# Performance work log

Hardware: AMD Instinct MI355X
Metric: run time of the kernel (lower is better)

Reference implementation:

```python
import jax, jax.numpy as jnp
import numpy as np


def _gcn_conv(x, src, dst, W, b, n_nodes):
    """PyG GCNConv: out = D^-1/2 (A+I) D^-1/2 (x @ W) + b, sym norm with self-loops."""
    loop = jnp.arange(n_nodes, dtype=src.dtype)
    s = jnp.concatenate([src, loop])  # sources incl self-loops
    d = jnp.concatenate([dst, loop])  # destinations incl self-loops
    ones = jnp.ones(d.shape[0], dtype=x.dtype)
    deg = jax.ops.segment_sum(ones, d, num_segments=n_nodes)
    dinv = jnp.where(deg > 0, jax.lax.rsqrt(deg), 0.0)
    norm = dinv[s] * dinv[d]  # [E+N]
    h = x @ W  # dense transform first (in>=out channels), [N, H]
    msg = h[s] * norm[:, None]  # gather + scale, [E+N, H]
    out = jax.ops.segment_sum(msg, d, num_segments=n_nodes)  # scatter-add
    return out + b


def setup_inputs() -> dict:
    N, E, C_IN, C_H = 50000, 640000, 128, 128
    key = jax.random.key(0)
    k_x, k_e, k_w1, k_w2 = jax.random.split(key, 4)
    x = jax.random.normal(k_x, (N, C_IN), dtype=jnp.float32)
    edge_index = jax.random.randint(k_e, (2, E), 0, N, dtype=jnp.int64)
    # Glorot-style init for GCN weights, zero bias (PyG defaults)
    W1 = jax.random.normal(k_w1, (C_IN, C_H), dtype=jnp.float32) * (1.0 / np.sqrt(C_IN))
    b1 = jnp.zeros((C_H,), dtype=jnp.float32)
    W2 = jax.random.normal(k_w2, (C_H, C_H), dtype=jnp.float32) * (1.0 / np.sqrt(C_H))
    b2 = jnp.zeros((C_H,), dtype=jnp.float32)
    return {"x": x, "edge_index": edge_index, "W1": W1, "b1": b1, "W2": W2, "b2": b2}


def reference(x, edge_index, W1, b1, W2, b2):
    n_nodes = x.shape[0]
    src, dst = edge_index[0], edge_index[1]
    h = jax.nn.relu(_gcn_conv(x, src, dst, W1, b1, n_nodes))
    # dropout p=0.5 is identity in eval mode (training=False)
    h = jax.nn.relu(_gcn_conv(h, src, dst, W2, b2, n_nodes))
    return h
```

## Files before the change

### kernel.cpp

```cpp
#include <hip/hip_runtime.h>
#include <hip/hip_bf16.h>
#include <cstdint>

#define CH 128
#define NB 512
#define SCHUNK 4096

typedef __attribute__((ext_vector_type(8))) short short8;
typedef __attribute__((ext_vector_type(4))) float f32x4;

union FragU {
  uint4 u;
  short8 s;
  ushort h[8];
};

__device__ __forceinline__ float bf_lo(uint32_t u) { return __uint_as_float(u << 16); }
__device__ __forceinline__ float bf_hi(uint32_t u) { return __uint_as_float(u & 0xffff0000u); }
__device__ __forceinline__ uint32_t f2bf(float f) {
  uint32_t u = __float_as_uint(f);
  u += 0x7fff + ((u >> 16) & 1);
  return u >> 16;
}

__global__ __launch_bounds__(256) void k_histw(const int* __restrict__ dst, int* __restrict__ counts,
                                               int E, int nblk,
                                               const float* __restrict__ W1, const float* __restrict__ W2,
                                               ushort* __restrict__ wbuf) {
  int blk = blockIdx.x;
  if (blk >= nblk) {
    int bb = blk - nblk;
    int which = bb >> 6;
    int idx = (bb & 63) * 256 + threadIdx.x;
    const float* W = which ? W2 : W1;
    ushort* hi = wbuf + which * 32768;
    ushort* lo = hi + 16384;
    int k = idx >> 7, n = idx & 127;
    float w = W[idx];
    uint32_t hb = f2bf(w);
    uint32_t lb = f2bf(w - bf_lo(hb));
    int j = n >> 4, t = k >> 5, ln = (n & 15) | (((k >> 3) & 3) << 4), i = k & 7;
    int p = (j * 4 + t) * 512 + ln * 8 + i;
    hi[p] = (ushort)hb;
    lo[p] = (ushort)lb;
    return;
  }
  __shared__ int sh[NB];
  int t = threadIdx.x;
  for (int i = t; i < NB; i += 256) sh[i] = 0;
  __syncthreads();
  int base = blk * SCHUNK, lim = min(base + SCHUNK, E);
  for (int i = base + t; i < lim; i += 256) atomicAdd(&sh[dst[i] >> 7], 1);
  __syncthreads();
  for (int i = t; i < NB; i += 256) counts[i * nblk + blk] = sh[i];
}

__global__ __launch_bounds__(1024) void k_scan1(const int* __restrict__ in, int* __restrict__ excl,
                                                int* __restrict__ blocksum, int n) {
  __shared__ int sd[1024];
  int tid = threadIdx.x;
  int i = blockIdx.x * 1024 + tid;
  int v = (i < n) ? in[i] : 0;
  int x = v;
  sd[tid] = x;
  __syncthreads();
  for (int off = 1; off < 1024; off <<= 1) {
    int t = (tid >= off) ? sd[tid - off] : 0;
    __syncthreads();
    x += t;
    sd[tid] = x;
    __syncthreads();
  }
  if (i < n) excl[i] = x - v;
  if (tid == 1023) blocksum[blockIdx.x] = x;
}

__global__ void k_scan2b(int* __restrict__ bs, int nb) {
  __shared__ int sh[128];
  int t = threadIdx.x;
  int v = (t < nb) ? bs[t] : 0;
  sh[t] = v;
  __syncthreads();
  for (int off = 1; off < 128; off <<= 1) {
    int add = (t >= off) ? sh[t - off] : 0;
    __syncthreads();
    sh[t] += add;
    __syncthreads();
  }
  if (t < nb) bs[t] = sh[t] - v;
}

__global__ __launch_bounds__(256) void k_scan3b(int* __restrict__ excl, const int* __restrict__ boff,
                                                int* __restrict__ bbase, int total, int nblk, int E) {
  int i = blockIdx.x * 256 + threadIdx.x;
  if (i < total) {
    int val = excl[i] + boff[i >> 10];
    excl[i] = val;
    if (i % nblk == 0) bbase[i / nblk] = val;
  }
  if (i == 0) bbase[NB] = E;
}

__global__ __launch_bounds__(256) void k_scatter3(const int* __restrict__ src, const int* __restrict__ dst,
                                                  const int* __restrict__ excl, uint32_t* __restrict__ packed,
                                                  int E, int nblk) {
  __shared__ int lcur[NB];
  int t = threadIdx.x, blk = blockIdx.x;
  for (int i = t; i < NB; i += 256) lcur[i] = excl[i * nblk + blk];
  __syncthreads();
  int base = blk * SCHUNK, lim = min(base + SCHUNK, E);
  for (int i = base + t; i < lim; i += 256) {
    int d = dst[i], s = src[i];
    int slot = atomicAdd(&lcur[d >> 7], 1);
    packed[slot] = (uint32_t)s | ((uint32_t)(d & 127) << 16);
  }
}

__global__ __launch_bounds__(256) void k_bucket(const uint32_t* __restrict__ packed, const int* __restrict__ bbase,
                                                int* __restrict__ csr_src, int* __restrict__ row_ptr,
                                                float* __restrict__ dinv, int N, int E, int nb) {
  __shared__ int hist[128];
  __shared__ int scan[128];
  __shared__ int cur[128];
  int b = blockIdx.x;
  int t = threadIdx.x;
  int base = bbase[b], end = bbase[b + 1];
  if (t < 128) hist[t] = 0;
  __syncthreads();
  for (int i = base + t; i < end; i += 256)
    atomicAdd(&hist[packed[i] >> 16], 1);
  __syncthreads();
  int v = (t < 128) ? hist[t] : 0;
  if (t < 128) scan[t] = v;
  __syncthreads();
  for (int off = 1; off < 128; off <<= 1) {
    int add = (t < 128 && t >= off) ? scan[t - off] : 0;
    __syncthreads();
    if (t < 128) scan[t] += add;
    __syncthreads();
  }
  if (t < 128) {
    int excl = scan[t] - v;
    cur[t] = excl;
    int node = b * 128 + t;
    if (node < N) {
      row_ptr[node] = base + excl;
      dinv[node] = rsqrtf((float)(v + 1));
    }
    if (b == nb - 1 && t == 0) row_ptr[N] = E;
  }
  __syncthreads();
  for (int i = base + t; i < end; i += 256) {
    uint32_t p = packed[i];
    int slot = atomicAdd(&cur[p >> 16], 1);
    csr_src[base + slot] = (int)(p & 0xffffu);
  }
}

__global__ __launch_bounds__(256) void k_gemm_mfma(const float* __restrict__ A,
                                                   const ushort* __restrict__ wpack,
                                                   const float* __restrict__ dinv,
                                                   ushort* __restrict__ Cp, int n) {
  const int lane = threadIdx.x & 63;
  const int gwave = (blockIdx.x * 256 + threadIdx.x) >> 6;
  const int rb = gwave * 32;
  if (rb >= n) return;
  const int lrow = lane & 15, lgrp = lane >> 4;
  const uint4* whi4 = (const uint4*)wpack;
  const uint4* wlo4 = (const uint4*)(wpack + 16384);

  const int r0 = rb + lrow, r1 = rb + 16 + lrow;
  const bool v0 = r0 < n, v1 = r1 < n;
  const int rc0 = v0 ? r0 : 0, rc1 = v1 ? r1 : 0;

  f32x4 acc0[8] = {};
  f32x4 acc1[8] = {};
  const uint4 zz = make_uint4(0, 0, 0, 0);

#pragma unroll
  for (int t = 0; t < 4; ++t) {
    FragU a0h, a0l, a1h, a1l;
    const float* ap0 = A + (size_t)rc0 * CH + t * 32 + lgrp * 8;
    const float* ap1 = A + (size_t)rc1 * CH + t * 32 + lgrp * 8;
    float4 xa = *(const float4*)ap0, xb = *(const float4*)(ap0 + 4);
    float4 ya = *(const float4*)ap1, yb = *(const float4*)(ap1 + 4);
    float xv[8] = {xa.x, xa.y, xa.z, xa.w, xb.x, xb.y, xb.z, xb.w};
    float yv[8] = {ya.x, ya.y, ya.z, ya.w, yb.x, yb.y, yb.z, yb.w};
#pragma unroll
    for (int i = 0; i < 8; ++i) {
      uint32_t h0 = f2bf(xv[i]);
      a0h.h[i] = (ushort)h0;
      a0l.h[i] = (ushort)f2bf(xv[i] - bf_lo(h0));
      uint32_t h1 = f2bf(yv[i]);
      a1h.h[i] = (ushort)h1;
      a1l.h[i] = (ushort)f2bf(yv[i] - bf_lo(h1));
    }
    if (!v0) { a0h.u = zz; a0l.u = zz; }
    if (!v1) { a1h.u = zz; a1l.u = zz; }
#pragma unroll
    for (int j = 0; j < 8; ++j) {
      FragU wh, wl;
      wh.u = whi4[(j * 4 + t) * 64 + lane];
      wl.u = wlo4[(j * 4 + t) * 64 + lane];
      acc0[j] = __builtin_amdgcn_mfma_f32_16x16x32_bf16(wh.s, a0h.s, acc0[j], 0, 0, 0);
      acc0[j] = __builtin_amdgcn_mfma_f32_16x16x32_bf16(wl.s, a0h.s, acc0[j], 0, 0, 0);
      acc0[j] = __builtin_amdgcn_mfma_f32_16x16x32_bf16(wh.s, a0l.s, acc0[j], 0, 0, 0);
      acc1[j] = __builtin_amdgcn_mfma_f32_16x16x32_bf16(wh.s, a1h.s, acc1[j], 0, 0, 0);
      acc1[j] = __builtin_amdgcn_mfma_f32_16x16x32_bf16(wl.s, a1h.s, acc1[j], 0, 0, 0);
      acc1[j] = __builtin_amdgcn_mfma_f32_16x16x32_bf16(wh.s, a1l.s, acc1[j], 0, 0, 0);
    }
  }

  if (v0) {
    float dv = dinv[r0];
#pragma unroll
    for (int j = 0; j < 8; ++j) {
      uint2 o;
      o.x = f2bf(acc0[j][0] * dv) | (f2bf(acc0[j][1] * dv) << 16);
      o.y = f2bf(acc0[j][2] * dv) | (f2bf(acc0[j][3] * dv) << 16);
      *(uint2*)&Cp[(size_t)r0 * CH + j * 16 + lgrp * 4] = o;
    }
  }
  if (v1) {
    float dv = dinv[r1];
#pragma unroll
    for (int j = 0; j < 8; ++j) {
      uint2 o;
      o.x = f2bf(acc1[j][0] * dv) | (f2bf(acc1[j][1] * dv) << 16);
      o.y = f2bf(acc1[j][2] * dv) | (f2bf(acc1[j][3] * dv) << 16);
      *(uint2*)&Cp[(size_t)r1 * CH + j * 16 + lgrp * 4] = o;
    }
  }
}

__device__ __forceinline__ void agg_node(const uint32_t* __restrict__ hp, const int* __restrict__ row_ptr,
                                         const int* __restrict__ csr, int v, int lane,
                                         float& a0, float& a1) {
  uint32_t self = hp[(size_t)v * 64 + lane];
  float acc0 = bf_lo(self), acc1 = bf_hi(self);
  int j = __builtin_amdgcn_readfirstlane(row_ptr[v]);
  int end = __builtin_amdgcn_readfirstlane(row_ptr[v + 1]);
  for (; j + 7 < end; j += 8) {
    int s[8];
#pragma unroll
    for (int k = 0; k < 8; ++k) s[k] = csr[j + k];
    uint32_t u[8];
#pragma unroll
    for (int k = 0; k < 8; ++k) u[k] = hp[(size_t)s[k] * 64 + lane];
#pragma unroll
    for (int k = 0; k < 8; ++k) { acc0 += bf_lo(u[k]); acc1 += bf_hi(u[k]); }
  }
  for (; j < end; ++j) {
    uint32_t u = hp[(size_t)csr[j] * 64 + lane];
    acc0 += bf_lo(u); acc1 += bf_hi(u);
  }
  a0 = acc0;
  a1 = acc1;
}

__global__ __launch_bounds__(256) void k_fused(const uint32_t* __restrict__ h1p, const int* __restrict__ row_ptr,
                                               const int* __restrict__ csr, const float* __restrict__ dinv,
                                               const float* __restrict__ b1,
                                               const ushort* __restrict__ wpack2,
                                               ushort* __restrict__ h2, int N) {
  __shared__ uint32_t sy[32 * 64];
  const int w = threadIdx.x >> 6;
  const int lane = threadIdx.x & 63;
  const int vb = blockIdx.x * 32;
  float2 bb = *(const float2*)&b1[2 * lane];

  for (int q = 0; q < 8; ++q) {
    int lv = w * 8 + q;
    int v = vb + lv;
    uint32_t packed = 0;
    if (v < N) {
      float a0, a1;
      agg_node(h1p, row_ptr, csr, v, lane, a0, a1);
      float dv = dinv[v];
      float o0 = fmaxf(fmaf(dv, a0, bb.x), 0.f);
      float o1 = fmaxf(fmaf(dv, a1, bb.y), 0.f);
      packed = f2bf(o0) | (f2bf(o1) << 16);
    }
    sy[lv * 64 + (lane ^ ((lv & 7) << 2))] = packed;
  }
  __syncthreads();

  const int lrow = lane & 15, lgrp = lane >> 4;
  const uint4* whi4 = (const uint4*)wpack2;
  const uint4* wlo4 = (const uint4*)(wpack2 + 16384);

  FragU af[2][4];
#pragma unroll
  for (int rt = 0; rt < 2; ++rt) {
#pragma unroll
    for (int t = 0; t < 4; ++t) {
      int row = rt * 16 + lrow;
      int grp = (t * 4 + lgrp) ^ (row & 7);
      af[rt][t].u = *(const uint4*)&sy[row * 64 + grp * 4];
    }
  }

  f32x4 acc[2][2] = {};
#pragma unroll
  for (int jj = 0; jj < 2; ++jj) {
    int j = w * 2 + jj;
#pragma unroll
    for (int t = 0; t < 4; ++t) {
      FragU wh, wl;
      wh.u = whi4[(j * 4 + t) * 64 + lane];
      wl.u = wlo4[(j * 4 + t) * 64 + lane];
      acc[0][jj] = __builtin_amdgcn_mfma_f32_16x16x32_bf16(wh.s, af[0][t].s, acc[0][jj], 0, 0, 0);
      acc[0][jj] = __builtin_amdgcn_mfma_f32_16x16x32_bf16(wl.s, af[0][t].s, acc[0][jj], 0, 0, 0);
      acc[1][jj] = __builtin_amdgcn_mfma_f32_16x16x32_bf16(wh.s, af[1][t].s, acc[1][jj], 0, 0, 0);
      acc[1][jj] = __builtin_amdgcn_mfma_f32_16x16x32_bf16(wl.s, af[1][t].s, acc[1][jj], 0, 0, 0);
    }
  }

#pragma unroll
  for (int rt = 0; rt < 2; ++rt) {
    int r = vb + rt * 16 + lrow;
    if (r < N) {
      float dvr = dinv[r];
#pragma unroll
      for (int jj = 0; jj < 2; ++jj) {
        int j = w * 2 + jj;
        uint2 o;
        o.x = f2bf(acc[rt][jj][0] * dvr) | (f2bf(acc[rt][jj][1] * dvr) << 16);
        o.y = f2bf(acc[rt][jj][2] * dvr) | (f2bf(acc[rt][jj][3] * dvr) << 16);
        *(uint2*)&h2[(size_t)r * CH + j * 16 + lgrp * 4] = o;
      }
    }
  }
}

__global__ __launch_bounds__(256) void k_agg2(const uint32_t* __restrict__ h2p, const int* __restrict__ row_ptr,
                                              const int* __restrict__ csr, const float* __restrict__ dinv,
                                              const float* __restrict__ b2, float* __restrict__ out, int n) {
  int v = (blockIdx.x * 256 + threadIdx.x) >> 6;
  int lane = threadIdx.x & 63;
  if (v >= n) return;
  v = __builtin_amdgcn_readfirstlane(v);
  float a0, a1;
  agg_node(h2p, row_ptr, csr, v, lane, a0, a1);
  float dv = dinv[v];
  float2 bb = *(const float2*)&b2[2 * lane];
  float o0 = fmaxf(fmaf(dv, a0, bb.x), 0.f);
  float o1 = fmaxf(fmaf(dv, a1, bb.y), 0.f);
  ((float2*)out)[(size_t)v * 64 + lane] = make_float2(o0, o1);
}


extern "C" void kernel_launch(void* const* d_in, const int* in_sizes, int n_in,
                              void* d_out, int out_size, void* d_ws, size_t ws_size,
                              hipStream_t stream) {
  const float* x  = (const float*)d_in[0];
  const int*   ei = (const int*)d_in[1];
  const float* W1 = (const float*)d_in[2];
  const float* b1 = (const float*)d_in[3];
  const float* W2 = (const float*)d_in[4];
  const float* b2 = (const float*)d_in[5];
  float* out = (float*)d_out;

  const int N = in_sizes[0] / CH;
  const int E = in_sizes[1] / 2;
  const int* src = ei;
  const int* dst = ei + E;
  const int nb = (N + 127) / 128;
  const int nblk = (E + SCHUNK - 1) / SCHUNK;
  const int total = NB * nblk;
  const int nsb = (total + 1023) / 1024;

  char* ws = (char*)d_ws;
  size_t off = 0;
  auto alloc = [&](size_t bytes) -> void* {
    void* p = ws + off;
    off += (bytes + 255) & ~(size_t)255;
    return p;
  };
  int*      counts  = (int*)alloc((size_t)total * 4);
  int*      blocksum= (int*)alloc(128 * 4);
  int*      bbase   = (int*)alloc((NB + 1) * 4);
  uint32_t* packed  = (uint32_t*)alloc((size_t)E * 4);
  int*      row_ptr = (int*)alloc((size_t)(N + 1) * 4);
  int*      csr_src = (int*)alloc((size_t)E * 4);
  float*    dinv    = (float*)alloc((size_t)N * 4);
  ushort*   wpack   = (ushort*)alloc(4 * 16384 * 2);
  ushort*   h1      = (ushort*)alloc((size_t)N * CH * 2);
  ushort*   h2      = (ushort*)alloc((size_t)N * CH * 2);
  (void)ws_size;

  k_histw<<<nblk + 128, 256, 0, stream>>>(dst, counts, E, nblk, W1, W2, wpack);
  k_scan1<<<nsb, 1024, 0, stream>>>(counts, counts, blocksum, total);
  k_scan2b<<<1, 128, 0, stream>>>(blocksum, nsb);
  k_scan3b<<<(total + 255) / 256, 256, 0, stream>>>(counts, blocksum, bbase, total, nblk, E);
  k_scatter3<<<nblk, 256, 0, stream>>>(src, dst, counts, packed, E, nblk);
  k_bucket<<<nb, 256, 0, stream>>>(packed, bbase, csr_src, row_ptr, dinv, N, E, nb);

  const int waves = (N + 31) / 32;
  const int gG = (waves + 3) / 4;
  const int gF = (N + 31) / 32;
  const int gA = (N + 3) / 4;

  k_gemm_mfma<<<gG, 256, 0, stream>>>(x, wpack, dinv, h1, N);
  k_fused<<<gF, 256, 0, stream>>>((const uint32_t*)h1, row_ptr, csr_src, dinv, b1,
                                  wpack + 32768, h2, N);
  k_agg2<<<gA, 256, 0, stream>>>((const uint32_t*)h2, row_ptr, csr_src, dinv, b2, out, N);
}
```

Measured before the change: 114.9 us.

## Split bf16 features into column halves for cache-friendly gather aggregation

Stores the intermediate bf16 feature matrices as two separate 64-column halves and aggregates each half in its own pass. Each wave processes two neighbor edges at once, one per 32-lane half, then combines them with a cross-lane shuffle. Layer 2 aggregation becomes two launches, one per half. The aim is to shrink the random-gather working set so it fits better in L2/MALL. The cost is reading the CSR indices twice, extra launches, and only half the lanes doing the writes.

```diff
diff --git a/kernel.cpp b/kernel.cpp
--- a/kernel.cpp
+++ b/kernel.cpp
@@ -160,7 +160,8 @@
 __global__ __launch_bounds__(256) void k_gemm_mfma(const float* __restrict__ A,
                                                    const ushort* __restrict__ wpack,
                                                    const float* __restrict__ dinv,
-                                                   ushort* __restrict__ Cp, int n) {
+                                                   ushort* __restrict__ Cl, ushort* __restrict__ Chh,
+                                                   int n) {
   const int lane = threadIdx.x & 63;
   const int gwave = (blockIdx.x * 256 + threadIdx.x) >> 6;
   const int rb = gwave * 32;
@@ -218,7 +219,8 @@
       uint2 o;
       o.x = f2bf(acc0[j][0] * dv) | (f2bf(acc0[j][1] * dv) << 16);
       o.y = f2bf(acc0[j][2] * dv) | (f2bf(acc0[j][3] * dv) << 16);
-      *(uint2*)&Cp[(size_t)r0 * CH + j * 16 + lgrp * 4] = o;
+      ushort* hp = (j < 4) ? Cl : Chh;
+      *(uint2*)&hp[(size_t)r0 * 64 + (j & 3) * 16 + lgrp * 4] = o;
     }
   }
   if (v1) {
@@ -228,60 +230,94 @@
       uint2 o;
       o.x = f2bf(acc1[j][0] * dv) | (f2bf(acc1[j][1] * dv) << 16);
       o.y = f2bf(acc1[j][2] * dv) | (f2bf(acc1[j][3] * dv) << 16);
-      *(uint2*)&Cp[(size_t)r1 * CH + j * 16 + lgrp * 4] = o;
-    }
-  }
-}
-
-__device__ __forceinline__ void agg_node(const uint32_t* __restrict__ hp, const int* __restrict__ row_ptr,
-                                         const int* __restrict__ csr, int v, int lane,
-                                         float& a0, float& a1) {
-  uint32_t self = hp[(size_t)v * 64 + lane];
-  float acc0 = bf_lo(self), acc1 = bf_hi(self);
+      ushort* hp = (j < 4) ? Cl : Chh;
+      *(uint2*)&hp[(size_t)r1 * 64 + (j & 3) * 16 + lgrp * 4] = o;
+    }
+  }
+}
+
+__device__ __forceinline__ void agg_half(const uint32_t* __restrict__ hh,
+                                         const int* __restrict__ row_ptr,
+                                         const int* __restrict__ csr,
+                                         int v, int hl, int eh,
+                                         float& r0, float& r1) {
+  float sel0 = (eh == 0) ? 1.f : 0.f;
+  uint32_t su = hh[(size_t)v * 32 + hl];
+  float a0 = bf_lo(su) * sel0, a1 = bf_hi(su) * sel0;
   int j = __builtin_amdgcn_readfirstlane(row_ptr[v]);
   int end = __builtin_amdgcn_readfirstlane(row_ptr[v + 1]);
-  for (; j + 7 < end; j += 8) {
-    int s[8];
-#pragma unroll
-    for (int k = 0; k < 8; ++k) s[k] = csr[j + k];
-    uint32_t u[8];
-#pragma unroll
-    for (int k = 0; k < 8; ++k) u[k] = hp[(size_t)s[k] * 64 + lane];
-#pragma unroll
-    for (int k = 0; k < 8; ++k) { acc0 += bf_lo(u[k]); acc1 += bf_hi(u[k]); }
-  }
-  for (; j < end; ++j) {
-    uint32_t u = hp[(size_t)csr[j] * 64 + lane];
-    acc0 += bf_lo(u); acc1 += bf_hi(u);
-  }
-  a0 = acc0;
-  a1 = acc1;
-}
-
-__global__ __launch_bounds__(256) void k_fused(const uint32_t* __restrict__ h1p, const int* __restrict__ row_ptr,
+  int cnt = end - j;
+  int npair = cnt >> 1;
+  int p = 0;
+  for (; p + 3 < npair; p += 4) {
+    int sE0 = csr[j + 2 * p + 0], sO0 = csr[j + 2 * p + 1];
+    int sE1 = csr[j + 2 * p + 2], sO1 = csr[j + 2 * p + 3];
+    int sE2 = csr[j + 2 * p + 4], sO2 = csr[j + 2 * p + 5];
+    int sE3 = csr[j + 2 * p + 6], sO3 = csr[j + 2 * p + 7];
+    int s0 = eh ? sO0 : sE0;
+    int s1 = eh ? sO1 : sE1;
+    int s2 = eh ? sO2 : sE2;
+    int s3 = eh ? sO3 : sE3;
+    uint32_t u0 = hh[(size_t)s0 * 32 + hl];
+    uint32_t u1 = hh[(size_t)s1 * 32 + hl];
+    uint32_t u2 = hh[(size_t)s2 * 32 + hl];
+    uint32_t u3 = hh[(size_t)s3 * 32 + hl];
+    a0 += bf_lo(u0); a1 += bf_hi(u0);
+    a0 += bf_lo(u1); a1 += bf_hi(u1);
+    a0 += bf_lo(u2); a1 += bf_hi(u2);
+    a0 += bf_lo(u3); a1 += bf_hi(u3);
+  }
+  for (; p < npair; ++p) {
+    int sE = csr[j + 2 * p], sO = csr[j + 2 * p + 1];
+    int s = eh ? sO : sE;
+    uint32_t u = hh[(size_t)s * 32 + hl];
+    a0 += bf_lo(u); a1 += bf_hi(u);
+  }
+  if (cnt & 1) {
+    int sT = __builtin_amdgcn_readfirstlane(csr[end - 1]);
+    uint32_t u = hh[(size_t)sT * 32 + hl];
+    a0 += bf_lo(u) * sel0; a1 += bf_hi(u) * sel0;
+  }
+  a0 += __shfl_xor(a0, 32, 64);
+  a1 += __shfl_xor(a1, 32, 64);
+  r0 = a0;
+  r1 = a1;
+}
+
+__global__ __launch_bounds__(256) void k_fused(const uint32_t* __restrict__ h1l, const uint32_t* __restrict__ h1h,
+                                               const int* __restrict__ row_ptr,
                                                const int* __restrict__ csr, const float* __restrict__ dinv,
                                                const float* __restrict__ b1,
                                                const ushort* __restrict__ wpack2,
-                                               ushort* __restrict__ h2, int N) {
+                                               ushort* __restrict__ h2l, ushort* __restrict__ h2h, int N) {
   __shared__ uint32_t sy[32 * 64];
   const int w = threadIdx.x >> 6;
   const int lane = threadIdx.x & 63;
+  const int hl = lane & 31;
+  const int eh = lane >> 5;
   const int vb = blockIdx.x * 32;
-  float2 bb = *(const float2*)&b1[2 * lane];
-
-  for (int q = 0; q < 8; ++q) {
-    int lv = w * 8 + q;
-    int v = vb + lv;
-    uint32_t packed = 0;
-    if (v < N) {
-      float a0, a1;
-      agg_node(h1p, row_ptr, csr, v, lane, a0, a1);
-      float dv = dinv[v];
-      float o0 = fmaxf(fmaf(dv, a0, bb.x), 0.f);
-      float o1 = fmaxf(fmaf(dv, a1, bb.y), 0.f);
-      packed = f2bf(o0) | (f2bf(o1) << 16);
-    }
-    sy[lv * 64 + (lane ^ ((lv & 7) << 2))] = packed;
+
+#pragma unroll
+  for (int ph = 0; ph < 2; ++ph) {
+    const uint32_t* hh = ph ? h1h : h1l;
+    float2 bb = *(const float2*)&b1[ph * 64 + 2 * hl];
+    for (int q = 0; q < 8; ++q) {
+      int lv = w * 8 + q;
+      int v = vb + lv;
+      uint32_t d = 0;
+      if (v < N) {
+        float a0, a1;
+        agg_half(hh, row_ptr, csr, v, hl, eh, a0, a1);
+        float dv = dinv[v];
+        float o0 = fmaxf(fmaf(dv, a0, bb.x), 0.f);
+        float o1 = fmaxf(fmaf(dv, a1, bb.y), 0.f);
+        d = f2bf(o0) | (f2bf(o1) << 16);
+      }
+      if (eh == 0) {
+        int widx = ph * 32 + hl;
+        sy[lv * 64 + (widx ^ ((lv & 7) << 2))] = d;
+      }
+    }
   }
   __syncthreads();
 
@@ -327,26 +363,31 @@
         uint2 o;
         o.x = f2bf(acc[rt][jj][0] * dvr) | (f2bf(acc[rt][jj][1] * dvr) << 16);
         o.y = f2bf(acc[rt][jj][2] * dvr) | (f2bf(acc[rt][jj][3] * dvr) << 16);
-        *(uint2*)&h2[(size_t)r * CH + j * 16 + lgrp * 4] = o;
+        ushort* hp = (j < 4) ? h2l : h2h;
+        *(uint2*)&hp[(size_t)r * 64 + (j & 3) * 16 + lgrp * 4] = o;
       }
     }
   }
 }
 
-__global__ __launch_bounds__(256) void k_agg2(const uint32_t* __restrict__ h2p, const int* __restrict__ row_ptr,
+template <int HALF>
+__global__ __launch_bounds__(256) void k_agg2(const uint32_t* __restrict__ hh, const int* __restrict__ row_ptr,
                                               const int* __restrict__ csr, const float* __restrict__ dinv,
                                               const float* __restrict__ b2, float* __restrict__ out, int n) {
-  int v = (blockIdx.x * 256 + threadIdx.x) >> 6;
+  int vw = (blockIdx.x * 256 + threadIdx.x) >> 6;
   int lane = threadIdx.x & 63;
-  if (v >= n) return;
-  v = __builtin_amdgcn_readfirstlane(v);
+  if (vw >= n) return;
+  int v = __builtin_amdgcn_readfirstlane(vw);
+  int hl = lane & 31;
+  int eh = lane >> 5;
   float a0, a1;
-  agg_node(h2p, row_ptr, csr, v, lane, a0, a1);
+  agg_half(hh, row_ptr, csr, v, hl, eh, a0, a1);
   float dv = dinv[v];
-  float2 bb = *(const float2*)&b2[2 * lane];
+  float2 bb = *(const float2*)&b2[HALF * 64 + 2 * hl];
   float o0 = fmaxf(fmaf(dv, a0, bb.x), 0.f);
   float o1 = fmaxf(fmaf(dv, a1, bb.y), 0.f);
-  ((float2*)out)[(size_t)v * 64 + lane] = make_float2(o0, o1);
+  if (eh == 0)
+    *(float2*)&out[(size_t)v * CH + HALF * 64 + 2 * hl] = make_float2(o0, o1);
 }
 
 
@@ -385,8 +426,10 @@
   int*      csr_src = (int*)alloc((size_t)E * 4);
   float*    dinv    = (float*)alloc((size_t)N * 4);
   ushort*   wpack   = (ushort*)alloc(4 * 16384 * 2);
-  ushort*   h1      = (ushort*)alloc((size_t)N * CH * 2);
-  ushort*   h2      = (ushort*)alloc((size_t)N * CH * 2);
+  ushort*   h1l     = (ushort*)alloc((size_t)N * 64 * 2);
+  ushort*   h1h     = (ushort*)alloc((size_t)N * 64 * 2);
+  ushort*   h2l     = (ushort*)alloc((size_t)N * 64 * 2);
+  ushort*   h2h     = (ushort*)alloc((size_t)N * 64 * 2);
   (void)ws_size;
 
   k_histw<<<nblk + 128, 256, 0, stream>>>(dst, counts, E, nblk, W1, W2, wpack);
@@ -401,8 +444,9 @@
   const int gF = (N + 31) / 32;
   const int gA = (N + 3) / 4;
 
-  k_gemm_mfma<<<gG, 256, 0, stream>>>(x, wpack, dinv, h1, N);
-  k_fused<<<gF, 256, 0, stream>>>((const uint32_t*)h1, row_ptr, csr_src, dinv, b1,
-                                  wpack + 32768, h2, N);
-  k_agg2<<<gA, 256, 0, stream>>>((const uint32_t*)h2, row_ptr, csr_src, dinv, b2, out, N);
-}
+  k_gemm_mfma<<<gG, 256, 0, stream>>>(x, wpack, dinv, h1l, h1h, N);
+  k_fused<<<gF, 256, 0, stream>>>((const uint32_t*)h1l, (const uint32_t*)h1h, row_ptr, csr_src,
+                                  dinv, b1, wpack + 32768, h2l, h2h, N);
+  k_agg2<0><<<gA, 256, 0, stream>>>((const uint32_t*)h2l, row_ptr, csr_src, dinv, b2, out, N);
+  k_agg2<1><<<gA, 256, 0, stream>>>((const uint32_t*)h2h, row_ptr, csr_src, dinv, b2, out, N);
+}
```

New measurement: 138.4 us. +20.4%, slower.
